# Kernel tuning notes

Hardware: AMD Instinct MI355X
Metric: run time of the kernel (lower is better)

## Reference

```python
import jax, jax.numpy as jnp
import numpy as np

THRESHOLD = 0.95


def setup_inputs() -> dict:
    key = jax.random.key(0)
    k1, k2 = jax.random.split(key, 2)
    B, T, D = 16, 2048, 1024
    hs = jax.random.normal(k1, (B, T, D), dtype=jnp.float32)
    hs_mask = jnp.ones((B, 1, T), dtype=jnp.float32)
    w = jax.random.normal(k2, (D,), dtype=jnp.float32) * 0.02  # project.weight [1,D] -> [D]
    b = jnp.zeros((), dtype=jnp.float32)                        # project.bias
    return {"hs": hs, "hs_mask": hs_mask, "w": w, "b": b}


def reference(hs, hs_mask, w, b):
    B, T, D = hs.shape
    # project + sigmoid + mask
    x = jnp.einsum("btd,d->bt", hs, w) + b            # [B,T]
    alphas_s = jax.nn.sigmoid(x)
    alphas = alphas_s * hs_mask[:, 0, :]              # [B,T]

    # ---- integrate-and-fire scan over time ----
    def step(carry, inp):
        integrate, frame = carry                      # [B], [B,D]
        alpha, h = inp                                # [B], [B,D]
        dist_completion = 1.0 - integrate
        integrate = integrate + alpha
        fire_val = integrate                          # recorded pre-reset value
        fireplace = integrate > THRESHOLD
        integrate = jnp.where(fireplace, integrate - 1.0, integrate)
        cur = jnp.where(fireplace, dist_completion, alpha)
        frame_out = frame + cur[:, None] * h          # recorded frame at t
        frame_next = jnp.where(fireplace[:, None], (alpha - cur)[:, None] * h, frame_out)
        return (integrate, frame_next), (fire_val, frame_out)

    init = (jnp.zeros((B,), hs.dtype), jnp.zeros((B, D), hs.dtype))
    _, (fires_t, frames_t) = jax.lax.scan(
        step, init, (jnp.swapaxes(alphas, 0, 1), jnp.swapaxes(hs, 0, 1)))
    fires = jnp.swapaxes(fires_t, 0, 1)               # [B,T]
    frames = jnp.swapaxes(frames_t, 0, 1)             # [B,T,D]

    # ---- gather fired frames, left-packed, padded to static L=T ----
    fired = fires > THRESHOLD                         # [B,T]
    pos = jnp.cumsum(fired.astype(jnp.int32), axis=1) - 1
    L = T                                             # static upper bound on label length
    pos = jnp.where(fired, pos, L)                    # out-of-range -> dropped
    bidx = jnp.broadcast_to(jnp.arange(B, dtype=jnp.int32)[:, None], (B, T))
    out = jnp.zeros((B, L, D), hs.dtype).at[bidx, pos].set(frames, mode="drop")

    len_labels = jnp.round(alphas.sum(-1)).astype(jnp.int32)          # [B]
    new_masks = (jnp.arange(L)[None, :] < len_labels[:, None])[:, None, :]  # [B,1,L] bool
    return out, new_masks
```

## Files before the change

kernel.cpp:

```cpp
#include <hip/hip_runtime.h>
#include <math.h>

#define BB 16
#define TT 2048
#define DD 1024
#define THRESH 0.95f
#define RPB 8

typedef float nt4 __attribute__((ext_vector_type(4)));

__device__ __forceinline__ void nt_store4(const float4& v, float4* p) {
    nt4 x = {v.x, v.y, v.z, v.w};
    __builtin_nontemporal_store(x, (nt4*)p);
}

__global__ __launch_bounds__(256) void proj_kernel(
    const float* __restrict__ hs, const float* __restrict__ hs_mask,
    const float* __restrict__ w, const float* __restrict__ bias,
    float* __restrict__ alphas)
{
    int row  = blockIdx.x * 4 + (threadIdx.x >> 6);
    int lane = threadIdx.x & 63;
    const float4* hp = (const float4*)(hs + (size_t)row * DD);
    const float4* wp = (const float4*)w;
    float sum = 0.f;
#pragma unroll
    for (int j = 0; j < 4; ++j) {
        float4 h4 = hp[lane + 64 * j];
        float4 w4 = wp[lane + 64 * j];
        sum += h4.x * w4.x + h4.y * w4.y + h4.z * w4.z + h4.w * w4.w;
    }
#pragma unroll
    for (int off = 32; off; off >>= 1) sum += __shfl_down(sum, off, 64);
    if (lane == 0) {
        float x  = sum + bias[0];
        float al = 1.f / (1.f + expf(-x));
        alphas[row] = al * hs_mask[row];
    }
}


#define SCAN_GROUP(RREG, GIDX)                                                \
    {                                                                         \
        float cv = 0.f, pv = 0.f;                                             \
        _Pragma("unroll 16")                                                  \
        for (int j = 0; j < 64; ++j) {                                        \
            float a = __int_as_float(                                         \
                __builtin_amdgcn_readlane(__float_as_int(RREG), j));          \
            float pre  = integ + a;                         \
            bool  fire = pre > THRESH;                      \
            float c    = fire ? dist : a;                                     \
            integ      = fire ? pre - 1.f : pre;        \
            dist       = 1.f - integ;                                         \
            bool sel   = (lane == j);                                         \
            cv = sel ? c   : cv;                                              \
            pv = sel ? pre : pv;                                              \
        }                                                                     \
        bool myfire = pv > THRESH;                                            \
        cp[(GIDX) * 64 + lane] = myfire ? -cv : cv;          \
        unsigned long long bm = __ballot(myfire);                             \
        gmask = (lane == (GIDX)) ? bm : gmask;                                \
    }

__global__ __launch_bounds__(64) void scan_kernel(
    const float* __restrict__ alphas, float* __restrict__ cur,
    int* __restrict__ fire_times, float* __restrict__ out_mask)
{
    int b    = blockIdx.x;
    int lane = threadIdx.x;
    const float* ap = alphas + (size_t)b * TT;
    float*       cp = cur    + (size_t)b * TT;

    unsigned long long gmask = 0ull;
    float integ = 0.f, dist = 1.f;
    double dsum = 0.0;

    for (int outer = 0; outer < 4; ++outer) {
        int base = outer * 512 + lane;
        float r0 = ap[base +   0];
        float r1 = ap[base +  64];
        float r2 = ap[base + 128];
        float r3 = ap[base + 192];
        float r4 = ap[base + 256];
        float r5 = ap[base + 320];
        float r6 = ap[base + 384];
        float r7 = ap[base + 448];
        dsum += (double)r0 + (double)r1 + (double)r2 + (double)r3
              + (double)r4 + (double)r5 + (double)r6 + (double)r7;
        int gb = outer * 8;
        SCAN_GROUP(r0, gb + 0)
        SCAN_GROUP(r1, gb + 1)
        SCAN_GROUP(r2, gb + 2)
        SCAN_GROUP(r3, gb + 3)
        SCAN_GROUP(r4, gb + 4)
        SCAN_GROUP(r5, gb + 5)
        SCAN_GROUP(r6, gb + 6)
        SCAN_GROUP(r7, gb + 7)
    }

#pragma unroll
    for (int off = 32; off; off >>= 1) dsum += __shfl_down(dsum, off, 64);
    int len = __double2int_rn(dsum);
    len = __shfl(len, 0, 64);
    float* mp = out_mask + (size_t)b * TT;
#pragma unroll
    for (int j = 0; j < TT / 64; ++j)
        mp[j * 64 + lane] = ((j * 64 + lane) < len) ? 1.f : 0.f;

    int cnt  = __popcll(gmask);
    int pref = cnt;
#pragma unroll
    for (int off = 1; off < 64; off <<= 1) {
        int y = __shfl_up(pref, off, 64);
        if (lane >= off) pref += y;
    }
    int pos = pref - cnt;
    unsigned long long m = gmask;
    int baset = lane * 64;
    int* fp = fire_times + (size_t)b * TT;
    while (m) {
        int j = __ffsll(m) - 1;
        fp[pos++] = baset + j;
        m &= m - 1;
    }

    int nf = __shfl(pref, 63, 64);
    int lastf = 0;
    if (nf > 0) lastf = fp[nf - 1];
    for (int r = nf + lane; r < TT; r += 64) fp[r] = lastf;
}

__global__ __launch_bounds__(256) void gather_kernel(
    const float* __restrict__ hs, const float* __restrict__ alphas,
    const float* __restrict__ cur, const int* __restrict__ fire_times,
    float* __restrict__ out)
{
    int chunk = blockIdx.x;
    int b  = chunk >> 8;
    int r0 = (chunk & 255) * RPB;
    int ti = threadIdx.x;

    const int*    ft  = fire_times + (size_t)b * TT;
    const float*  al  = alphas     + (size_t)b * TT;
    const float*  cu  = cur        + (size_t)b * TT;
    const float4* hsb = (const float4*)(hs + (size_t)b * TT * DD);
    float4*       ob  = (float4*)(out + ((size_t)b * TT + r0) * DD);

    int t1 = ft[r0 + RPB - 1];
    int t;
    float4 acc = {0.f, 0.f, 0.f, 0.f};
    if (r0 == 0) {
        t = 0;
    } else {
        int   tp = ft[r0 - 1];
        float cr = cu[tp];
        float wb = al[tp] - fabsf(cr);
        float4 h = hsb[(size_t)tp * 256 + ti];
        acc.x = wb * h.x; acc.y = wb * h.y;
        acc.z = wb * h.z; acc.w = wb * h.w;
        t = tp + 1;
    }

    int emitted = 0;
#pragma unroll 2
    for (; t <= t1; ++t) {
        float  cr = cu[t];
        float4 h  = hsb[(size_t)t * 256 + ti];
        float  cw = fabsf(cr);
        acc.x += cw * h.x; acc.y += cw * h.y;
        acc.z += cw * h.z; acc.w += cw * h.w;
        if (cr < 0.f) {
            nt_store4(acc, &ob[(size_t)emitted * 256 + ti]);
            float wb = al[t] - cw;
            acc.x = wb * h.x; acc.y = wb * h.y;
            acc.z = wb * h.z; acc.w = wb * h.w;
            ++emitted;
        }
    }

    float4 z = {0.f, 0.f, 0.f, 0.f};
    for (int i = emitted; i < RPB; ++i)
        nt_store4(z, &ob[(size_t)i * 256 + ti]);
}

extern "C" void kernel_launch(void* const* d_in, const int* in_sizes, int n_in,
                              void* d_out, int out_size, void* d_ws, size_t ws_size,
                              hipStream_t stream) {
    const float* hs      = (const float*)d_in[0];
    const float* hs_mask = (const float*)d_in[1];
    const float* w       = (const float*)d_in[2];
    const float* bias    = (const float*)d_in[3];

    float* out      = (float*)d_out;
    float* out_mask = out + (size_t)BB * TT * DD;

    float* alphas     = (float*)d_ws;
    float* cur        = alphas + BB * TT;
    int*   fire_times = (int*)(cur + BB * TT);

    proj_kernel<<<BB * TT / 4, 256, 0, stream>>>(hs, hs_mask, w, bias, alphas);
    scan_kernel<<<BB, 64, 0, stream>>>(alphas, cur, fire_times, out_mask);
    gather_kernel<<<BB * (TT / RPB), 256, 0, stream>>>(hs, alphas, cur,
                                                       fire_times, out);
}
```

Baseline: 304.8 us.

## Fuse projection and scan via last-block-done atomic counter per batch

Merges the projection kernel and the per-batch scan kernel into one launch. Each block computes four alphas, then bumps a per-batch atomic counter, and the last block for a batch runs the scan on the alphas already in global memory. This removes one kernel launch boundary and lets scans for early batches overlap with projection of later batches. In exchange it adds a memset launch, atomics and fences, and the scan still runs on a single wave per batch.

Result: slower. 680.3 us (+123.1%).

```diff
diff --git a/kernel.cpp b/kernel.cpp
--- a/kernel.cpp
+++ b/kernel.cpp
@@ -13,32 +13,6 @@
     nt4 x = {v.x, v.y, v.z, v.w};
     __builtin_nontemporal_store(x, (nt4*)p);
 }
-
-__global__ __launch_bounds__(256) void proj_kernel(
-    const float* __restrict__ hs, const float* __restrict__ hs_mask,
-    const float* __restrict__ w, const float* __restrict__ bias,
-    float* __restrict__ alphas)
-{
-    int row  = blockIdx.x * 4 + (threadIdx.x >> 6);
-    int lane = threadIdx.x & 63;
-    const float4* hp = (const float4*)(hs + (size_t)row * DD);
-    const float4* wp = (const float4*)w;
-    float sum = 0.f;
-#pragma unroll
-    for (int j = 0; j < 4; ++j) {
-        float4 h4 = hp[lane + 64 * j];
-        float4 w4 = wp[lane + 64 * j];
-        sum += h4.x * w4.x + h4.y * w4.y + h4.z * w4.z + h4.w * w4.w;
-    }
-#pragma unroll
-    for (int off = 32; off; off >>= 1) sum += __shfl_down(sum, off, 64);
-    if (lane == 0) {
-        float x  = sum + bias[0];
-        float al = 1.f / (1.f + expf(-x));
-        alphas[row] = al * hs_mask[row];
-    }
-}
-
 
 #define SCAN_GROUP(RREG, GIDX)                                                \
     {                                                                         \
@@ -62,12 +36,47 @@
         gmask = (lane == (GIDX)) ? bm : gmask;                                \
     }
 
-__global__ __launch_bounds__(64) void scan_kernel(
-    const float* __restrict__ alphas, float* __restrict__ cur,
-    int* __restrict__ fire_times, float* __restrict__ out_mask)
+__global__ __launch_bounds__(256) void proj_scan_kernel(
+    const float* __restrict__ hs, const float* __restrict__ hs_mask,
+    const float* __restrict__ w, const float* __restrict__ bias,
+    float* __restrict__ alphas, float* __restrict__ cur,
+    int* __restrict__ fire_times, float* __restrict__ out_mask,
+    int* __restrict__ done_ctr)
 {
-    int b    = blockIdx.x;
-    int lane = threadIdx.x;
+    __shared__ int s_last;
+    int row  = blockIdx.x * 4 + (threadIdx.x >> 6);
+    int lane = threadIdx.x & 63;
+    int b    = blockIdx.x >> 9;
+
+    {
+        const float4* hp = (const float4*)(hs + (size_t)row * DD);
+        const float4* wp = (const float4*)w;
+        float sum = 0.f;
+#pragma unroll
+        for (int j = 0; j < 4; ++j) {
+            float4 h4 = hp[lane + 64 * j];
+            float4 w4 = wp[lane + 64 * j];
+            sum += h4.x * w4.x + h4.y * w4.y + h4.z * w4.z + h4.w * w4.w;
+        }
+#pragma unroll
+        for (int off = 32; off; off >>= 1) sum += __shfl_down(sum, off, 64);
+        if (lane == 0) {
+            float x  = sum + bias[0];
+            float al = 1.f / (1.f + expf(-x));
+            __hip_atomic_store(&alphas[row], al * hs_mask[row],
+                               __ATOMIC_RELAXED, __HIP_MEMORY_SCOPE_AGENT);
+        }
+    }
+
+    __syncthreads();
+    if (threadIdx.x == 0) {
+        __threadfence();
+        int old = atomicAdd(&done_ctr[b], 1);
+        s_last = (old == 511);
+    }
+    __syncthreads();
+    if (!s_last || threadIdx.x >= 64) return;
+
     const float* ap = alphas + (size_t)b * TT;
     float*       cp = cur    + (size_t)b * TT;
 
@@ -77,14 +86,14 @@
 
     for (int outer = 0; outer < 4; ++outer) {
         int base = outer * 512 + lane;
-        float r0 = ap[base +   0];
-        float r1 = ap[base +  64];
-        float r2 = ap[base + 128];
-        float r3 = ap[base + 192];
-        float r4 = ap[base + 256];
-        float r5 = ap[base + 320];
-        float r6 = ap[base + 384];
-        float r7 = ap[base + 448];
+        float r0 = __hip_atomic_load(&ap[base +   0], __ATOMIC_RELAXED, __HIP_MEMORY_SCOPE_AGENT);
+        float r1 = __hip_atomic_load(&ap[base +  64], __ATOMIC_RELAXED, __HIP_MEMORY_SCOPE_AGENT);
+        float r2 = __hip_atomic_load(&ap[base + 128], __ATOMIC_RELAXED, __HIP_MEMORY_SCOPE_AGENT);
+        float r3 = __hip_atomic_load(&ap[base + 192], __ATOMIC_RELAXED, __HIP_MEMORY_SCOPE_AGENT);
+        float r4 = __hip_atomic_load(&ap[base + 256], __ATOMIC_RELAXED, __HIP_MEMORY_SCOPE_AGENT);
+        float r5 = __hip_atomic_load(&ap[base + 320], __ATOMIC_RELAXED, __HIP_MEMORY_SCOPE_AGENT);
+        float r6 = __hip_atomic_load(&ap[base + 384], __ATOMIC_RELAXED, __HIP_MEMORY_SCOPE_AGENT);
+        float r7 = __hip_atomic_load(&ap[base + 448], __ATOMIC_RELAXED, __HIP_MEMORY_SCOPE_AGENT);
         dsum += (double)r0 + (double)r1 + (double)r2 + (double)r3
               + (double)r4 + (double)r5 + (double)r6 + (double)r7;
         int gb = outer * 8;
@@ -197,9 +206,13 @@
     float* alphas     = (float*)d_ws;
     float* cur        = alphas + BB * TT;
     int*   fire_times = (int*)(cur + BB * TT);
-
-    proj_kernel<<<BB * TT / 4, 256, 0, stream>>>(hs, hs_mask, w, bias, alphas);
-    scan_kernel<<<BB, 64, 0, stream>>>(alphas, cur, fire_times, out_mask);
+    int*   done_ctr   = fire_times + BB * TT;
+
+    hipMemsetAsync(done_ctr, 0, BB * sizeof(int), stream);
+
+    proj_scan_kernel<<<BB * TT / 4, 256, 0, stream>>>(hs, hs_mask, w, bias,
+                                                      alphas, cur, fire_times,
+                                                      out_mask, done_ctr);
     gather_kernel<<<BB * (TT / RPB), 256, 0, stream>>>(hs, alphas, cur,
                                                        fire_times, out);
 }
```
